# Performance work log

Hardware: AMD Instinct MI355X
Metric: run time of the kernel (lower is better)

Reference implementation:

```python
import jax, jax.numpy as jnp
import numpy as np
import math

B, C, W, H = 4, 96, 64, 64
MID, OUT = 24, 256
EPS = 1e-5


def setup_inputs() -> dict:
    key = jax.random.key(0)
    ks = jax.random.split(key, 8)
    s = lambda *sh: 1.0 / math.sqrt(sh[-1])
    return {
        "rgb": jax.random.normal(ks[0], (B, C, W, H), dtype=jnp.float32),
        "dep": jax.random.normal(ks[1], (B, C, W, H), dtype=jnp.float32),
        "Wd": jax.random.normal(ks[2], (C, C), dtype=jnp.float32) * s(C, C),   # dept 1x1 conv
        "Wr": jax.random.normal(ks[3], (C, C), dtype=jnp.float32) * s(C, C),   # rgb 1x1 conv
        "Wm1": jax.random.normal(ks[4], (MID, C), dtype=jnp.float32) * s(MID, C),
        "bn1_g": jnp.ones((MID,), dtype=jnp.float32),
        "bn1_b": jnp.zeros((MID,), dtype=jnp.float32),
        "Wm2": jax.random.normal(ks[5], (OUT, MID), dtype=jnp.float32) * s(OUT, MID),
        "bn2_g": jnp.ones((OUT,), dtype=jnp.float32),
        "bn2_b": jnp.zeros((OUT,), dtype=jnp.float32),
    }


def _bn_relu(x, gamma, beta):
    # training-mode BatchNorm over batch dim (spatial is 1x1), biased variance, then ReLU
    mu = x.mean(axis=0)
    var = x.var(axis=0)
    y = (x - mu) * jax.lax.rsqrt(var + EPS) * gamma + beta
    return jax.nn.relu(y)


def reference(rgb, dep, Wd, Wr, Wm1, bn1_g, bn1_b, Wm2, bn2_g, bn2_b):
    b, c, w, h = rgb.shape
    hw = w * h
    rgbd = rgb + dep
    # 1x1 convs as channel matmuls -> [B, C, HW]
    pr = jnp.einsum('oc,bchw->bohw', Wr, rgb).reshape(b, c, hw)
    pd = jnp.einsum('oc,bchw->bohw', Wd, dep).reshape(b, c, hw)
    # energy[b, n, m] = proj_rgb^T proj_dep / sqrt(C)   -> [B, HW, HW]
    energy = jnp.einsum('bcn,bcm->bnm', pr, pd) / math.sqrt(c)
    # torch Softmax(dim=1) on [B, HW, HW] normalizes over the first HW axis
    att = jax.nn.softmax(energy, axis=1)
    att_r = jnp.einsum('bcn,bnm->bcm', pr, att)
    att_b = jnp.einsum('bcn,bnm->bcm', pd, att)
    out = (att_r + att_b).reshape(b, c, w, h) + rgbd
    gap = out.mean(axis=(2, 3))  # [B, C] (AdaptiveAvgPool2d(1) squeezed)
    h1 = _bn_relu(gap @ Wm1.T, bn1_g, bn1_b)        # [B, 24]
    gate = _bn_relu(h1 @ Wm2.T, bn2_g, bn2_b)       # [B, OUT] (ReLU, as in source)
    return gate[:, :, None, None]                    # [B, OUT, 1, 1]
```

## Files before the change

### kernel.cpp

```cpp
#include <hip/hip_runtime.h>

#define HW 4096
#define NC 96
#define NB 4
#define MID 24
#define NOUT 256
#define BEPS 1e-5f
#define SCALE_E 0.10206207261596575f

typedef unsigned short u16;
typedef short bf16x8 __attribute__((ext_vector_type(8)));
typedef unsigned short u16x8 __attribute__((ext_vector_type(8)));
typedef float f32x16 __attribute__((ext_vector_type(16)));

__device__ __forceinline__ u16 bfh(float x) {
  unsigned u = __float_as_uint(x);
  return (u16)((u + 0x7FFFu + ((u >> 16) & 1u)) >> 16);
}

__launch_bounds__(256)
__global__ void k_prep(const float* __restrict__ rgb, const float* __restrict__ dep,
                       const float* __restrict__ Wr, const float* __restrict__ Wd,
                       float* __restrict__ psum, u16* __restrict__ prF, u16* __restrict__ pdF) {
  const int tid = threadIdx.x;
  const int lane = tid & 63;
  const int og = __builtin_amdgcn_readfirstlane(tid >> 6);
  const int b = blockIdx.y, q = blockIdx.z;
  const int n0 = blockIdx.x * 64;
  const int n = n0 + lane;
  const int obase = q * 32 + og * 8;

  float ar[8], ad[8];
  #pragma unroll
  for (int o = 0; o < 8; ++o) { ar[o] = 0.f; ad[o] = 0.f; }

  const float* rb = rgb + (size_t)b * NC * HW + n;
  const float* db = dep + (size_t)b * NC * HW + n;
  #pragma unroll 4
  for (int c = 0; c < NC; ++c) {
    float xr = rb[(size_t)c * HW];
    float xd = db[(size_t)c * HW];
    #pragma unroll
    for (int o = 0; o < 8; ++o) {
      float wr = Wr[(obase + o) * NC + c];
      float wd = Wd[(obase + o) * NC + c];
      ar[o] = fmaf(wr, xr, ar[o]);
      ad[o] = fmaf(wd, xd, ad[o]);
    }
  }

  #pragma unroll
  for (int o = 0; o < 8; ++o)
    psum[((size_t)b * NC + obase + o) * HW + n] = ar[o] + ad[o];

  const int c8 = q * 4 + og;
  const int ks = c8 >> 1, khalf = c8 & 1;
  const int tile = n >> 5;
  const size_t off = (size_t)b * HW * 96
                   + ((size_t)(tile * 6 + ks) << 9) + ((khalf * 32 + (n & 31)) << 3);
  u16x8 vr, vd;
  #pragma unroll
  for (int o = 0; o < 8; ++o) { vr[o] = bfh(ar[o]); vd[o] = bfh(ad[o]); }
  *(u16x8*)(prF + off) = vr;
  *(u16x8*)(pdF + off) = vd;
}

template <int PASS>
__launch_bounds__(256, 2)
__global__ void k_energy(const u16* __restrict__ At, const u16* __restrict__ Bt,
                         const float* __restrict__ zin, float* __restrict__ part) {
  __shared__ float red[2][128];
  __shared__ float nlzL[128];
  const int tid = threadIdx.x;
  const int lane = tid & 63, wid = tid >> 6;
  const int wA = wid >> 1, wB = wid & 1;
  const int b = blockIdx.z;
  const int flat = blockIdx.y * 32 + blockIdx.x;
  const int by = (flat & 7) * 4 + ((flat >> 3) & 3);
  const int bx = flat >> 5;
  const int a0 = by * 128;
  const int c0 = bx * 128;
  const u16* Ab = At + (size_t)b * HW * 96;
  const u16* Bb = Bt + (size_t)b * HW * 96;
  const int tA0 = by * 4 + wA * 2;
  const int tB0 = bx * 4 + wB * 2;

  if (PASS) {
    if (tid < 128) {
      float s = 0.f;
      #pragma unroll
      for (int t = 0; t < 32; ++t) s += zin[((size_t)t * NB + b) * HW + a0 + tid];
      nlzL[tid] = -__logf(s);
    }
    __syncthreads();
  }

  bf16x8 Ah[2][6];
  #pragma unroll
  for (int ta = 0; ta < 2; ++ta)
    #pragma unroll
    for (int ks = 0; ks < 6; ++ks)
      Ah[ta][ks] = *(const bf16x8*)(Ab + (((tA0 + ta) * 6 + ks) << 9) + (lane << 3));

  f32x16 acc[2][2];
  #pragma unroll
  for (int ta = 0; ta < 2; ++ta)
    #pragma unroll
    for (int tb = 0; tb < 2; ++tb)
      #pragma unroll
      for (int q = 0; q < 16; ++q) acc[ta][tb][q] = 0.f;

  #pragma unroll
  for (int ks = 0; ks < 6; ++ks) {
    #pragma unroll
    for (int tb = 0; tb < 2; ++tb) {
      bf16x8 bh = *(const bf16x8*)(Bb + (((tB0 + tb) * 6 + ks) << 9) + (lane << 3));
      #pragma unroll
      for (int ta = 0; ta < 2; ++ta)
        acc[ta][tb] = __builtin_amdgcn_mfma_f32_32x32x16_bf16(Ah[ta][ks], bh, acc[ta][tb], 0, 0, 0);
    }
  }

  float csum[2] = {0.f, 0.f};
  float nlzv = 0.f;
  if (PASS) nlzv = nlzL[wA * 64 + lane];
  #pragma unroll
  for (int ta = 0; ta < 2; ++ta) {
    #pragma unroll
    for (int q = 0; q < 16; ++q) {
      float bias = 0.f;
      if (PASS) {
        int src = ta * 32 + (q & 3) + 8 * (q >> 2) + 4 * (lane >> 5);
        bias = __shfl(nlzv, src, 64);
      }
      #pragma unroll
      for (int tb = 0; tb < 2; ++tb)
        csum[tb] += __expf(fmaf(acc[ta][tb][q], SCALE_E, bias));
    }
  }
  #pragma unroll
  for (int tb = 0; tb < 2; ++tb) csum[tb] += __shfl_xor(csum[tb], 32, 64);
  if (lane < 32) {
    #pragma unroll
    for (int tb = 0; tb < 2; ++tb) red[wA][wB * 64 + tb * 32 + lane] = csum[tb];
  }
  __syncthreads();
  if (tid < 128)
    part[((size_t)by * NB + b) * HW + c0 + tid] = red[0][tid] + red[1][tid];
}

__global__ void k_sred(const float* __restrict__ spart, float* __restrict__ sv) {
  int idx = blockIdx.x * 256 + threadIdx.x;
  float a = 0.f;
  #pragma unroll
  for (int t = 0; t < 32; ++t) a += spart[(size_t)t * (NB * HW) + idx];
  sv[idx] = a;
}

__launch_bounds__(256)
__global__ void k_gap(const float* __restrict__ psum, const float* __restrict__ rgb,
                      const float* __restrict__ dep, const float* __restrict__ sv,
                      float* __restrict__ gap) {
  const int c = blockIdx.x, b = blockIdx.y;
  const size_t off = ((size_t)b * NC + c) * HW;
  const float* pp = psum + off;
  const float* rp = rgb + off;
  const float* dp = dep + off;
  const float* sp = sv + (size_t)b * HW;
  float a1 = 0.f, a2 = 0.f;
  for (int n = threadIdx.x * 4; n < HW; n += 1024) {
    float4 p = *(const float4*)&pp[n];
    float4 s4 = *(const float4*)&sp[n];
    float4 r4 = *(const float4*)&rp[n];
    float4 d4 = *(const float4*)&dp[n];
    a1 += p.x * s4.x + p.y * s4.y + p.z * s4.z + p.w * s4.w;
    a2 += (r4.x + d4.x) + (r4.y + d4.y) + (r4.z + d4.z) + (r4.w + d4.w);
  }
  #pragma unroll
  for (int o = 32; o > 0; o >>= 1) {
    a1 += __shfl_down(a1, o, 64);
    a2 += __shfl_down(a2, o, 64);
  }
  __shared__ float r1[4], r2[4];
  const int wv = threadIdx.x >> 6;
  if ((threadIdx.x & 63) == 0) { r1[wv] = a1; r2[wv] = a2; }
  __syncthreads();
  if (threadIdx.x == 0) {
    float t1 = r1[0] + r1[1] + r1[2] + r1[3];
    float t2 = r2[0] + r2[1] + r2[2] + r2[3];
    gap[b * NC + c] = (t1 + t2) * (1.0f / HW);
  }
}

__launch_bounds__(256)
__global__ void k_mlp(const float* __restrict__ gap,
                      const float* __restrict__ Wm1, const float* __restrict__ g1,
                      const float* __restrict__ b1,
                      const float* __restrict__ Wm2, const float* __restrict__ g2,
                      const float* __restrict__ b2, float* __restrict__ out) {
  __shared__ float gl[NB * NC];
  __shared__ float h[NB * MID];
  __shared__ float h1r[NB * MID];
  __shared__ float h2[NB * NOUT];
  const int tid = threadIdx.x;
  for (int i = tid; i < NB * NC; i += 256) gl[i] = gap[i];
  __syncthreads();

  if (tid < NB * MID) {
    int b = tid / MID, j = tid % MID;
    float acc = 0.f;
    #pragma unroll
    for (int c = 0; c < NC; ++c) acc += gl[b * NC + c] * Wm1[j * NC + c];
    h[b * MID + j] = acc;
  }
  __syncthreads();

  if (tid < MID) {
    float x0 = h[0 * MID + tid], x1 = h[1 * MID + tid];
    float x2 = h[2 * MID + tid], x3 = h[3 * MID + tid];
    float mu = 0.25f * (x0 + x1 + x2 + x3);
    float d0 = x0 - mu, d1 = x1 - mu, d2 = x2 - mu, d3 = x3 - mu;
    float v = 0.25f * (d0 * d0 + d1 * d1 + d2 * d2 + d3 * d3);
    float sc = g1[tid] * rsqrtf(v + BEPS);
    float bb = b1[tid];
    h1r[0 * MID + tid] = fmaxf(d0 * sc + bb, 0.f);
    h1r[1 * MID + tid] = fmaxf(d1 * sc + bb, 0.f);
    h1r[2 * MID + tid] = fmaxf(d2 * sc + bb, 0.f);
    h1r[3 * MID + tid] = fmaxf(d3 * sc + bb, 0.f);
  }
  __syncthreads();

  for (int idx = tid; idx < NB * NOUT; idx += 256) {
    int b = idx >> 8, o = idx & 255;
    float acc = 0.f;
    #pragma unroll
    for (int j = 0; j < MID; ++j) acc += h1r[b * MID + j] * Wm2[o * MID + j];
    h2[b * NOUT + o] = acc;
  }
  __syncthreads();

  if (tid < NOUT) {
    float x0 = h2[0 * NOUT + tid], x1 = h2[1 * NOUT + tid];
    float x2 = h2[2 * NOUT + tid], x3 = h2[3 * NOUT + tid];
    float mu = 0.25f * (x0 + x1 + x2 + x3);
    float d0 = x0 - mu, d1 = x1 - mu, d2 = x2 - mu, d3 = x3 - mu;
    float v = 0.25f * (d0 * d0 + d1 * d1 + d2 * d2 + d3 * d3);
    float sc = g2[tid] * rsqrtf(v + BEPS);
    float bb = b2[tid];
    out[0 * NOUT + tid] = fmaxf(d0 * sc + bb, 0.f);
    out[1 * NOUT + tid] = fmaxf(d1 * sc + bb, 0.f);
    out[2 * NOUT + tid] = fmaxf(d2 * sc + bb, 0.f);
    out[3 * NOUT + tid] = fmaxf(d3 * sc + bb, 0.f);
  }
}

extern "C" void kernel_launch(void* const* d_in, const int* in_sizes, int n_in,
                              void* d_out, int out_size, void* d_ws, size_t ws_size,
                              hipStream_t stream) {
  const float* rgb   = (const float*)d_in[0];
  const float* dep   = (const float*)d_in[1];
  const float* Wd    = (const float*)d_in[2];
  const float* Wr    = (const float*)d_in[3];
  const float* Wm1   = (const float*)d_in[4];
  const float* bn1_g = (const float*)d_in[5];
  const float* bn1_b = (const float*)d_in[6];
  const float* Wm2   = (const float*)d_in[7];
  const float* bn2_g = (const float*)d_in[8];
  const float* bn2_b = (const float*)d_in[9];
  float* out = (float*)d_out;

  char* w = (char*)d_ws;
  u16* prF = (u16*)w;             w += (size_t)NB * HW * 96 * 2;
  u16* pdF = (u16*)w;             w += (size_t)NB * HW * 96 * 2;
  float* psum  = (float*)w;       w += (size_t)NB * NC * HW * 4;
  float* zpart = (float*)w;       w += (size_t)32 * NB * HW * 4;
  float* spart = (float*)w;       w += (size_t)32 * NB * HW * 4;
  float* sv    = (float*)w;       w += (size_t)NB * HW * 4;
  float* gap   = (float*)w;       w += (size_t)NB * NC * 4;

  k_prep<<<dim3(HW / 64, NB, 3), 256, 0, stream>>>(rgb, dep, Wr, Wd, psum, prF, pdF);
  k_energy<0><<<dim3(32, 32, NB), 256, 0, stream>>>(prF, pdF, nullptr, zpart);
  k_energy<1><<<dim3(32, 32, NB), 256, 0, stream>>>(pdF, prF, zpart, spart);
  k_sred<<<NB * HW / 256, 256, 0, stream>>>(spart, sv);
  k_gap<<<dim3(NC, NB), 256, 0, stream>>>(psum, rgb, dep, sv, gap);
  k_mlp<<<1, 256, 0, stream>>>(gap, Wm1, bn1_g, bn1_b, Wm2, bn2_g, bn2_b, out);
}
```

Baseline: 84.97 us.

## Accumulate softmax partials atomically, fuse GAP with MLP, use exp2 scaling

The energy kernels now atomically add their column partial sums directly into Z and sv instead of writing 32-way partial buffers, so the k_sred kernel and the per-row 32-way reduction in pass 1 go away. The GAP kernel absorbs the MLP tail through a last-block-done counter, which removes one launch. The softmax exponent is rewritten as exp2 with a log2e-folded scale. In exchange, two memsets are added, summation order becomes nondeterministic, and there is atomic contention on 16K addresses.

```diff
diff --git a/kernel.cpp b/kernel.cpp
--- a/kernel.cpp
+++ b/kernel.cpp
@@ -6,7 +6,7 @@
 #define MID 24
 #define NOUT 256
 #define BEPS 1e-5f
-#define SCALE_E 0.10206207261596575f
+#define SCALE2E 0.14724920341279385f
 
 typedef unsigned short u16;
 typedef short bf16x8 __attribute__((ext_vector_type(8)));
@@ -26,8 +26,7 @@
   const int lane = tid & 63;
   const int og = __builtin_amdgcn_readfirstlane(tid >> 6);
   const int b = blockIdx.y, q = blockIdx.z;
-  const int n0 = blockIdx.x * 64;
-  const int n = n0 + lane;
+  const int n = blockIdx.x * 64 + lane;
   const int obase = q * 32 + og * 8;
 
   float ar[8], ad[8];
@@ -68,7 +67,7 @@
 template <int PASS>
 __launch_bounds__(256, 2)
 __global__ void k_energy(const u16* __restrict__ At, const u16* __restrict__ Bt,
-                         const float* __restrict__ zin, float* __restrict__ part) {
+                         const float* __restrict__ Zin, float* __restrict__ outv) {
   __shared__ float red[2][128];
   __shared__ float nlzL[128];
   const int tid = threadIdx.x;
@@ -86,12 +85,8 @@
   const int tB0 = bx * 4 + wB * 2;
 
   if (PASS) {
-    if (tid < 128) {
-      float s = 0.f;
-      #pragma unroll
-      for (int t = 0; t < 32; ++t) s += zin[((size_t)t * NB + b) * HW + a0 + tid];
-      nlzL[tid] = -__logf(s);
-    }
+    if (tid < 128)
+      nlzL[tid] = -__log2f(Zin[(size_t)b * HW + a0 + tid]);
     __syncthreads();
   }
 
@@ -135,7 +130,7 @@
       }
       #pragma unroll
       for (int tb = 0; tb < 2; ++tb)
-        csum[tb] += __expf(fmaf(acc[ta][tb][q], SCALE_E, bias));
+        csum[tb] += exp2f(fmaf(acc[ta][tb][q], SCALE2E, bias));
     }
   }
   #pragma unroll
@@ -146,29 +141,26 @@
   }
   __syncthreads();
   if (tid < 128)
-    part[((size_t)by * NB + b) * HW + c0 + tid] = red[0][tid] + red[1][tid];
-}
-
-__global__ void k_sred(const float* __restrict__ spart, float* __restrict__ sv) {
-  int idx = blockIdx.x * 256 + threadIdx.x;
-  float a = 0.f;
-  #pragma unroll
-  for (int t = 0; t < 32; ++t) a += spart[(size_t)t * (NB * HW) + idx];
-  sv[idx] = a;
+    atomicAdd(&outv[(size_t)b * HW + c0 + tid], red[0][tid] + red[1][tid]);
 }
 
 __launch_bounds__(256)
 __global__ void k_gap(const float* __restrict__ psum, const float* __restrict__ rgb,
                       const float* __restrict__ dep, const float* __restrict__ sv,
-                      float* __restrict__ gap) {
+                      float* __restrict__ gapb, int* __restrict__ counter,
+                      const float* __restrict__ Wm1, const float* __restrict__ g1,
+                      const float* __restrict__ b1,
+                      const float* __restrict__ Wm2, const float* __restrict__ g2,
+                      const float* __restrict__ b2, float* __restrict__ out) {
   const int c = blockIdx.x, b = blockIdx.y;
+  const int tid = threadIdx.x;
   const size_t off = ((size_t)b * NC + c) * HW;
   const float* pp = psum + off;
   const float* rp = rgb + off;
   const float* dp = dep + off;
   const float* sp = sv + (size_t)b * HW;
   float a1 = 0.f, a2 = 0.f;
-  for (int n = threadIdx.x * 4; n < HW; n += 1024) {
+  for (int n = tid * 4; n < HW; n += 1024) {
     float4 p = *(const float4*)&pp[n];
     float4 s4 = *(const float4*)&sp[n];
     float4 r4 = *(const float4*)&rp[n];
@@ -182,36 +174,36 @@
     a2 += __shfl_down(a2, o, 64);
   }
   __shared__ float r1[4], r2[4];
-  const int wv = threadIdx.x >> 6;
-  if ((threadIdx.x & 63) == 0) { r1[wv] = a1; r2[wv] = a2; }
-  __syncthreads();
-  if (threadIdx.x == 0) {
+  __shared__ int isLast;
+  const int wv = tid >> 6;
+  if ((tid & 63) == 0) { r1[wv] = a1; r2[wv] = a2; }
+  __syncthreads();
+  if (tid == 0) {
     float t1 = r1[0] + r1[1] + r1[2] + r1[3];
     float t2 = r2[0] + r2[1] + r2[2] + r2[3];
-    gap[b * NC + c] = (t1 + t2) * (1.0f / HW);
-  }
-}
-
-__launch_bounds__(256)
-__global__ void k_mlp(const float* __restrict__ gap,
-                      const float* __restrict__ Wm1, const float* __restrict__ g1,
-                      const float* __restrict__ b1,
-                      const float* __restrict__ Wm2, const float* __restrict__ g2,
-                      const float* __restrict__ b2, float* __restrict__ out) {
+    gapb[b * NC + c] = (t1 + t2) * (1.0f / HW);
+    __threadfence();
+    int old = atomicAdd(counter, 1);
+    isLast = (old == NC * NB - 1);
+  }
+  __syncthreads();
+  if (!isLast) return;
+
   __shared__ float gl[NB * NC];
   __shared__ float h[NB * MID];
   __shared__ float h1r[NB * MID];
   __shared__ float h2[NB * NOUT];
-  const int tid = threadIdx.x;
-  for (int i = tid; i < NB * NC; i += 256) gl[i] = gap[i];
+  __threadfence();
+  for (int i = tid; i < NB * NC; i += 256)
+    gl[i] = atomicAdd(&gapb[i], 0.0f);
   __syncthreads();
 
   if (tid < NB * MID) {
-    int b = tid / MID, j = tid % MID;
+    int bb2 = tid / MID, j = tid % MID;
     float acc = 0.f;
     #pragma unroll
-    for (int c = 0; c < NC; ++c) acc += gl[b * NC + c] * Wm1[j * NC + c];
-    h[b * MID + j] = acc;
+    for (int cc = 0; cc < NC; ++cc) acc += gl[bb2 * NC + cc] * Wm1[j * NC + cc];
+    h[bb2 * MID + j] = acc;
   }
   __syncthreads();
 
@@ -231,11 +223,11 @@
   __syncthreads();
 
   for (int idx = tid; idx < NB * NOUT; idx += 256) {
-    int b = idx >> 8, o = idx & 255;
+    int bb2 = idx >> 8, o = idx & 255;
     float acc = 0.f;
     #pragma unroll
-    for (int j = 0; j < MID; ++j) acc += h1r[b * MID + j] * Wm2[o * MID + j];
-    h2[b * NOUT + o] = acc;
+    for (int j = 0; j < MID; ++j) acc += h1r[bb2 * MID + j] * Wm2[o * MID + j];
+    h2[bb2 * NOUT + o] = acc;
   }
   __syncthreads();
 
@@ -272,16 +264,18 @@
   char* w = (char*)d_ws;
   u16* prF = (u16*)w;             w += (size_t)NB * HW * 96 * 2;
   u16* pdF = (u16*)w;             w += (size_t)NB * HW * 96 * 2;
-  float* psum  = (float*)w;       w += (size_t)NB * NC * HW * 4;
-  float* zpart = (float*)w;       w += (size_t)32 * NB * HW * 4;
-  float* spart = (float*)w;       w += (size_t)32 * NB * HW * 4;
-  float* sv    = (float*)w;       w += (size_t)NB * HW * 4;
-  float* gap   = (float*)w;       w += (size_t)NB * NC * 4;
+  float* psum = (float*)w;        w += (size_t)NB * NC * HW * 4;
+  float* Z    = (float*)w;        w += (size_t)NB * HW * 4;
+  float* sv   = (float*)w;        w += (size_t)NB * HW * 4;
+  float* gap  = (float*)w;        w += (size_t)NB * NC * 4;
+  int* counter = (int*)w;         w += 256;
+
+  hipMemsetAsync(Z, 0, (size_t)NB * HW * 4 * 2, stream);
+  hipMemsetAsync(counter, 0, 4, stream);
 
   k_prep<<<dim3(HW / 64, NB, 3), 256, 0, stream>>>(rgb, dep, Wr, Wd, psum, prF, pdF);
-  k_energy<0><<<dim3(32, 32, NB), 256, 0, stream>>>(prF, pdF, nullptr, zpart);
-  k_energy<1><<<dim3(32, 32, NB), 256, 0, stream>>>(pdF, prF, zpart, spart);
-  k_sred<<<NB * HW / 256, 256, 0, stream>>>(spart, sv);
-  k_gap<<<dim3(NC, NB), 256, 0, stream>>>(psum, rgb, dep, sv, gap);
-  k_mlp<<<1, 256, 0, stream>>>(gap, Wm1, bn1_g, bn1_b, Wm2, bn2_g, bn2_b, out);
-}
+  k_energy<0><<<dim3(32, 32, NB), 256, 0, stream>>>(prF, pdF, nullptr, Z);
+  k_energy<1><<<dim3(32, 32, NB), 256, 0, stream>>>(pdF, prF, Z, sv);
+  k_gap<<<dim3(NC, NB), 256, 0, stream>>>(psum, rgb, dep, sv, gap, counter,
+                                          Wm1, bn1_g, bn1_b, Wm2, bn2_g, bn2_b, out);
+}
```

New measurement: 105.4 us. 24.0% more time.
